# Optimization experiments

Measured on AMD Instinct MI355X. Metric: run time of the kernel, lower is better.

Reference implementation:

```python
import jax, jax.numpy as jnp
import numpy as np

B, S, H = 2, 2048, 1024
G, HEADS = 4, 16
HPG = HEADS // G          # heads per group = 4
HD = H // HEADS           # head_dim = 64
DG = H // G               # per-group proj dim = 256
SCALE = 1.0 / np.sqrt(HD)


def setup_inputs() -> dict:
    key = jax.random.key(0)
    ks = jax.random.split(key, 6)
    w = 0.02
    return {
        "hidden_states": jax.random.normal(ks[0], (B, S, H), dtype=jnp.float32),
        "Wq": jax.random.normal(ks[1], (G, DG, H), dtype=jnp.float32) * w,
        "bq": jnp.zeros((G, DG), dtype=jnp.float32),
        "Wk": jax.random.normal(ks[2], (G, DG, H), dtype=jnp.float32) * w,
        "bk": jnp.zeros((G, DG), dtype=jnp.float32),
        "Wv": jax.random.normal(ks[3], (G, DG, H), dtype=jnp.float32) * w,
        "bv": jnp.zeros((G, DG), dtype=jnp.float32),
        "Wo": jax.random.normal(ks[4], (H, H), dtype=jnp.float32) * w,
        "bo": jnp.zeros((H,), dtype=jnp.float32),
    }


def _proj_split(x, W, b):
    # x: [B,S,H], W: [G,DG,H], b: [G,DG] -> [B,G,HPG,S,HD]
    y = jnp.einsum("bsh,gdh->bgsd", x, W) + b[None, :, None, :]
    y = y.reshape(x.shape[0], G, x.shape[1], HPG, HD)
    return jnp.transpose(y, (0, 1, 3, 2, 4))


def reference(hidden_states, Wq, bq, Wk, bk, Wv, bv, Wo, bo):
    q = _proj_split(hidden_states, Wq, bq)  # [B,G,HPG,S,HD]
    k = _proj_split(hidden_states, Wk, bk)
    v = _proj_split(hidden_states, Wv, bv)
    scores = jnp.einsum("bghqd,bghkd->bghqk", q, k) * SCALE
    attn = jax.nn.softmax(scores.astype(jnp.float32), axis=-1).astype(v.dtype)
    ctx = jnp.einsum("bghqk,bghkd->bghqd", attn, v)  # [B,G,HPG,S,HD]
    # merge: heads ordered group-major, matching torch cat over group dim
    ctx = jnp.transpose(ctx, (0, 3, 1, 2, 4)).reshape(hidden_states.shape[0], hidden_states.shape[1], H)
    return jnp.einsum("bsh,oh->bso", ctx, Wo) + bo
```

## Files before the change

### kernel.cpp

```cpp
#include <hip/hip_runtime.h>

typedef __bf16 bf16x8 __attribute__((ext_vector_type(8)));
typedef float f32x4 __attribute__((ext_vector_type(4)));
typedef float f32x16 __attribute__((ext_vector_type(16)));
typedef unsigned int uint4v __attribute__((ext_vector_type(4)));
typedef unsigned int uint2v __attribute__((ext_vector_type(2)));

#define LOG2E 1.4426950408889634f

static __device__ __forceinline__ unsigned short f2bf(float f) {
  union { float f; unsigned int u; } c; c.f = f;
  return (unsigned short)((c.u + 0x7fffu + ((c.u >> 16) & 1u)) >> 16);
}

static __device__ __forceinline__ void gload16(const void* g, void* l) {
  __builtin_amdgcn_global_load_lds(
      (const __attribute__((address_space(1))) void*)g,
      (__attribute__((address_space(3))) void*)l, 16, 0, 0);
}

static __device__ __forceinline__ float exp2fast(float x) {
#if __has_builtin(__builtin_amdgcn_exp2f)
  return __builtin_amdgcn_exp2f(x);
#else
  return exp2f(x);
#endif
}

static __device__ __forceinline__ f32x16 mfma32(bf16x8 a, bf16x8 b, f32x16 c) {
  return __builtin_amdgcn_mfma_f32_32x32x16_bf16(a, b, c, 0, 0, 0);
}

static __device__ __forceinline__ unsigned cvt_pk_bf16(float a, float b) {
  unsigned r;
  asm("v_cvt_pk_bf16_f32 %0, %1, %2" : "=v"(r) : "v"(a), "v"(b));
  return r;
}

static __device__ __forceinline__ void pl32_swap(unsigned& a, unsigned& b) {
#if __has_builtin(__builtin_amdgcn_permlane32_swap)
  uint2v r = __builtin_amdgcn_permlane32_swap(a, b, false, false);
  a = r[0]; b = r[1];
#else
  asm volatile("v_permlane32_swap_b32 %0, %1" : "+v"(a), "+v"(b));
#endif
}

__global__ void cvt_all(const float* __restrict__ x,
                        const float* __restrict__ Wq,
                        const float* __restrict__ Wk,
                        const float* __restrict__ Wv,
                        const float* __restrict__ Wo,
                        ushort4* __restrict__ dst) {
  int i = blockIdx.x * 256 + threadIdx.x;
  const float* src;
  int off;
  if (i < 1048576) {
    src = x; off = i;
  } else {
    int t = (i - 1048576) >> 18;
    off = (i - 1048576) & 262143;
    src = (t == 0) ? Wq : (t == 1) ? Wk : (t == 2) ? Wv : Wo;
  }
  float4 f = ((const float4*)src)[off];
  ushort4 o;
  o.x = f2bf(f.x); o.y = f2bf(f.y); o.z = f2bf(f.z); o.w = f2bf(f.w);
  dst[i] = o;
}

__launch_bounds__(256, 4)
__global__ void qkv_gemm(const unsigned short* __restrict__ xb,
                         const unsigned short* __restrict__ wq,
                         const unsigned short* __restrict__ wk,
                         const unsigned short* __restrict__ wv,
                         const float* __restrict__ bq,
                         const float* __restrict__ bk,
                         const float* __restrict__ bv,
                         unsigned short* __restrict__ Qo,
                         unsigned short* __restrict__ Ko,
                         unsigned short* __restrict__ VTo) {
  __shared__ unsigned short As[128 * 64];
  __shared__ unsigned short Bs[128 * 64];
  const int s0 = blockIdx.x * 128;
  const int n0g = blockIdx.y * 128;
  const int qkv = n0g >> 10;
  const int d0 = n0g & 1023;
  const unsigned short* W = (qkv == 0) ? wq : ((qkv == 1) ? wk : wv);
  const float* bias = (qkv == 0) ? bq : ((qkv == 1) ? bk : bv);

  const unsigned short* Aptr; const unsigned short* Bptr;
  int Aoff, Boff;
  if (qkv < 2) { Aptr = W;  Aoff = d0; Bptr = xb; Boff = s0; }
  else         { Aptr = xb; Aoff = s0; Bptr = W;  Boff = d0; }

  const int tid = threadIdx.x;
  const int lane = tid & 63;
  const int wid = tid >> 6;
  const int wm = (wid >> 1) * 64;
  const int wn = (wid & 1) * 64;
  const int lm = lane & 15;
  const int quad = lane >> 4;

  f32x4 acc[4][4] = {};

  for (int kk = 0; kk < 1024; kk += 64) {
#pragma unroll
    for (int t = 0; t < 4; ++t) {
      int i = t * 256 + tid;
      int row = i >> 3, tp = i & 7;
      int seg = tp ^ (row & 7);
      gload16(Aptr + (size_t)(Aoff + row) * 1024 + kk + seg * 8,
              As + (size_t)i * 8);
      gload16(Bptr + (size_t)(Boff + row) * 1024 + kk + seg * 8,
              Bs + (size_t)i * 8);
    }
    __syncthreads();
#pragma unroll
    for (int h = 0; h < 2; ++h) {
      bf16x8 af[4], bff[4];
#pragma unroll
      for (int mt = 0; mt < 4; ++mt) {
        int r = wm + mt * 16 + lm;
        af[mt] = *(const bf16x8*)(As + r * 64 + (((h * 4 + quad) ^ (r & 7)) * 8));
      }
#pragma unroll
      for (int nt = 0; nt < 4; ++nt) {
        int r = wn + nt * 16 + lm;
        bff[nt] = *(const bf16x8*)(Bs + r * 64 + (((h * 4 + quad) ^ (r & 7)) * 8));
      }
#pragma unroll
      for (int mt = 0; mt < 4; ++mt)
#pragma unroll
        for (int nt = 0; nt < 4; ++nt)
          acc[mt][nt] = __builtin_amdgcn_mfma_f32_16x16x32_bf16(
              af[mt], bff[nt], acc[mt][nt], 0, 0, 0);
    }
    __syncthreads();
  }

  if (qkv < 2) {
    unsigned short* OUT = (qkv == 0) ? Qo : Ko;
    const float scale = (qkv == 0) ? (0.125f * LOG2E) : 1.0f;
#pragma unroll
    for (int mt = 0; mt < 4; ++mt) {
      const int d = d0 + wm + mt * 16 + quad * 4;
      const int g = d >> 8, hpg = (d >> 6) & 3, hd = d & 63;
      const float4 bb = *(const float4*)(bias + d);
#pragma unroll
      for (int nt = 0; nt < 4; ++nt) {
        const int srow = s0 + wn + nt * 16 + lm;
        const int bidx = srow >> 11, s = srow & 2047;
        const int head = (bidx * 4 + g) * 4 + hpg;
        ushort4 o;
        o.x = f2bf((acc[mt][nt][0] + bb.x) * scale);
        o.y = f2bf((acc[mt][nt][1] + bb.y) * scale);
        o.z = f2bf((acc[mt][nt][2] + bb.z) * scale);
        o.w = f2bf((acc[mt][nt][3] + bb.w) * scale);
        *(ushort4*)(OUT + (size_t)head * 131072 + (size_t)s * 64 + hd) = o;
      }
    }
  } else {
#pragma unroll
    for (int nt = 0; nt < 4; ++nt) {
      const int d = d0 + wn + nt * 16 + lm;
      const int g = d >> 8, hpg = (d >> 6) & 3, hd = d & 63;
      const float bb = bias[d];
#pragma unroll
      for (int mt = 0; mt < 4; ++mt) {
        const int sbase = s0 + wm + mt * 16 + quad * 4;
        const int bidx = sbase >> 11, s = sbase & 2047;
        const int head = (bidx * 4 + g) * 4 + hpg;
        ushort4 o;
        o.x = f2bf(acc[mt][nt][0] + bb);
        o.y = f2bf(acc[mt][nt][1] + bb);
        o.z = f2bf(acc[mt][nt][2] + bb);
        o.w = f2bf(acc[mt][nt][3] + bb);
        *(ushort4*)(VTo + (size_t)head * 131072 + (size_t)hd * 2048 + s) = o;
      }
    }
  }
}

static __device__ __forceinline__ void stage_kv(
    const unsigned short* Kh, const unsigned short* Vh, int kv0,
    unsigned short* ksl, unsigned short* vsl, int tid) {
#pragma unroll
  for (int t = 0; t < 4; ++t) {
    int i = t * 256 + tid;
    int r = i >> 3, j = i & 7;
    gload16(Kh + (size_t)(kv0 + r) * 64 + ((j ^ (r & 7)) << 3),
            ksl + (size_t)i * 8);
  }
#pragma unroll
  for (int t = 0; t < 4; ++t) {
    int i = t * 256 + tid;
    int r = i >> 4, j = i & 15;
    gload16(Vh + (size_t)r * 2048 + kv0 + ((j ^ (r & 15)) << 3),
            vsl + (size_t)i * 8);
  }
}

__launch_bounds__(256, 2)
__global__ void attn_kernel(const unsigned short* __restrict__ Q,
                            const unsigned short* __restrict__ K,
                            const unsigned short* __restrict__ VT,
                            unsigned short* __restrict__ ctx) {
  __shared__ __align__(16) unsigned char smem[65536];

  const int f = blockIdx.x;
  const int xcd = f & 7;
  const int idx = f >> 3;
  const int head = xcd * 4 + (idx & 3);
  const int q0 = (idx >> 2) * 128;
  const int b = head >> 4;
  const int colbase = (head & 15) * 64;

  const unsigned short* Qh = Q + (size_t)head * 131072;
  const unsigned short* Kh = K + (size_t)head * 131072;
  const unsigned short* Vh = VT + (size_t)head * 131072;

  const int tid = threadIdx.x;
  const int lane = tid & 63;
  const int w = tid >> 6;
  const int wq = w & 1;
  const int wkv = w >> 1;
  const int l31 = lane & 31;
  const int hi = lane >> 5;

  stage_kv(Kh, Vh, 0, (unsigned short*)smem,
           (unsigned short*)(smem + 32768), tid);

  bf16x8 qf[2][4];
#pragma unroll
  for (int qs = 0; qs < 2; ++qs) {
    const size_t qrow = (size_t)(q0 + wq * 64 + qs * 32 + l31);
#pragma unroll
    for (int s = 0; s < 4; ++s)
      qf[qs][s] = *(const bf16x8*)(Qh + qrow * 64 + s * 16 + hi * 8);
  }

  int koff[2][4];
#pragma unroll
  for (int kb = 0; kb < 2; ++kb) {
    const int row = wkv * 64 + kb * 32 + l31;
#pragma unroll
    for (int s = 0; s < 4; ++s) {
      const int c = s * 2 + hi;
      koff[kb][s] = row * 64 + ((c ^ (row & 7)) << 3);
    }
  }
  int voff[2][2][2];
#pragma unroll
  for (int kb = 0; kb < 2; ++kb)
#pragma unroll
    for (int db = 0; db < 2; ++db) {
      const int row = db * 32 + l31;
#pragma unroll
      for (int t = 0; t < 2; ++t) {
        const int c = wkv * 8 + kb * 4 + t * 2 + hi;
        voff[kb][db][t] = row * 128 + ((c ^ (row & 15)) << 3);
      }
    }

  __syncthreads();

  float psum[2] = {0.f, 0.f};
  f32x16 oacc[2][2] = {};

  for (int it = 0; it < 16; ++it) {
    const int buf = it & 1;
    const unsigned short* kbuf = (const unsigned short*)(smem + buf * 16384);
    const unsigned short* vbuf =
        (const unsigned short*)(smem + 32768 + buf * 16384);
    if (it < 15)
      stage_kv(Kh, Vh, (it + 1) * 128,
               (unsigned short*)(smem + (buf ^ 1) * 16384),
               (unsigned short*)(smem + 32768 + (buf ^ 1) * 16384), tid);

#pragma unroll
    for (int kb = 0; kb < 2; ++kb) {
      bf16x8 kf[4], vf[2][2];
#pragma unroll
      for (int s = 0; s < 4; ++s)
        kf[s] = *(const bf16x8*)(kbuf + koff[kb][s]);
#pragma unroll
      for (int db = 0; db < 2; ++db)
#pragma unroll
        for (int t = 0; t < 2; ++t)
          vf[db][t] = *(const bf16x8*)(vbuf + voff[kb][db][t]);

#pragma unroll
      for (int qs = 0; qs < 2; ++qs) {
        f32x16 sc = {};
#pragma unroll
        for (int s = 0; s < 4; ++s)
          sc = mfma32(kf[s], qf[qs][s], sc);

        float e[16];
#pragma unroll
        for (int r = 0; r < 16; ++r) e[r] = exp2fast(sc[r]);
        {
          float t0 = (e[0] + e[1]) + (e[2] + e[3]);
          float t1 = (e[4] + e[5]) + (e[6] + e[7]);
          float t2 = (e[8] + e[9]) + (e[10] + e[11]);
          float t3 = (e[12] + e[13]) + (e[14] + e[15]);
          psum[qs] += (t0 + t1) + (t2 + t3);
        }
        unsigned p[8];
#pragma unroll
        for (int j = 0; j < 8; ++j) p[j] = cvt_pk_bf16(e[2 * j], e[2 * j + 1]);
        pl32_swap(p[0], p[2]); pl32_swap(p[1], p[3]);
        pl32_swap(p[4], p[6]); pl32_swap(p[5], p[7]);
        uint4v u0 = {p[0], p[1], p[2], p[3]};
        uint4v u1 = {p[4], p[5], p[6], p[7]};
        const bf16x8 B0 = __builtin_bit_cast(bf16x8, u0);
        const bf16x8 B1 = __builtin_bit_cast(bf16x8, u1);
#pragma unroll
        for (int db = 0; db < 2; ++db) {
          oacc[qs][db] = mfma32(vf[db][0], B0, oacc[qs][db]);
          oacc[qs][db] = mfma32(vf[db][1], B1, oacc[qs][db]);
        }
      }
    }
    __syncthreads();
  }

#pragma unroll
  for (int qs = 0; qs < 2; ++qs)
    psum[qs] += __shfl_xor(psum[qs], 32, 64);

  float* red = (float*)smem;
  float* psred = (float*)(smem + 34816);
  if (wkv == 1) {
#pragma unroll
    for (int qs = 0; qs < 2; ++qs) {
      const int qi = wq * 64 + qs * 32 + l31;
      if (hi == 0) psred[qi] = psum[qs];
#pragma unroll
      for (int db = 0; db < 2; ++db)
#pragma unroll
        for (int g = 0; g < 4; ++g) {
          f32x4 ov;
          ov[0] = oacc[qs][db][4 * g + 0];
          ov[1] = oacc[qs][db][4 * g + 1];
          ov[2] = oacc[qs][db][4 * g + 2];
          ov[3] = oacc[qs][db][4 * g + 3];
          *(f32x4*)(red + qi * 68 + db * 32 + g * 8 + hi * 4) = ov;
        }
    }
  }
  __syncthreads();
  if (wkv == 0) {
#pragma unroll
    for (int qs = 0; qs < 2; ++qs) {
      const int qi = wq * 64 + qs * 32 + l31;
      const float inv = 1.0f / (psum[qs] + psred[qi]);
      const size_t row = (size_t)(b * 2048 + q0 + qi);
#pragma unroll
      for (int db = 0; db < 2; ++db)
#pragma unroll
        for (int g = 0; g < 4; ++g) {
          f32x4 o = *(const f32x4*)(red + qi * 68 + db * 32 + g * 8 + hi * 4);
          ushort4 st;
          st.x = f2bf((o[0] + oacc[qs][db][4 * g + 0]) * inv);
          st.y = f2bf((o[1] + oacc[qs][db][4 * g + 1]) * inv);
          st.z = f2bf((o[2] + oacc[qs][db][4 * g + 2]) * inv);
          st.w = f2bf((o[3] + oacc[qs][db][4 * g + 3]) * inv);
          *(ushort4*)(ctx + row * 1024 + colbase + db * 32 + g * 8 + hi * 4) =
              st;
        }
    }
  }
}

__launch_bounds__(256, 4)
__global__ void out_gemm(const unsigned short* __restrict__ A,
                         const unsigned short* __restrict__ Wb,
                         const float* __restrict__ bo,
                         float* __restrict__ out) {
  __shared__ unsigned short As[128 * 64];
  __shared__ unsigned short Bs[64 * 64];
  const int s0 = blockIdx.x * 64;
  const int o0 = blockIdx.y * 128;

  const int tid = threadIdx.x;
  const int lane = tid & 63;
  const int wid = tid >> 6;
  const int wm = (wid >> 1) * 64;
  const int wn = (wid & 1) * 32;
  const int lm = lane & 15;
  const int quad = lane >> 4;

  f32x4 acc[4][2] = {};

  for (int kk = 0; kk < 1024; kk += 64) {
#pragma unroll
    for (int t = 0; t < 4; ++t) {
      int i = t * 256 + tid;
      int row = i >> 3, tp = i & 7;
      int seg = tp ^ (row & 7);
      gload16(Wb + (size_t)(o0 + row) * 1024 + kk + seg * 8, As + (size_t)i * 8);
    }
#pragma unroll
    for (int t = 0; t < 2; ++t) {
      int i = t * 256 + tid;
      int row = i >> 3, tp = i & 7;
      int seg = tp ^ (row & 7);
      gload16(A + (size_t)(s0 + row) * 1024 + kk + seg * 8, Bs + (size_t)i * 8);
    }
    __syncthreads();
#pragma unroll
    for (int h = 0; h < 2; ++h) {
      bf16x8 af[4], bff[2];
#pragma unroll
      for (int mt = 0; mt < 4; ++mt) {
        int r = wm + mt * 16 + lm;
        af[mt] = *(const bf16x8*)(As + r * 64 + (((h * 4 + quad) ^ (r & 7)) * 8));
      }
#pragma unroll
      for (int nt = 0; nt < 2; ++nt) {
        int r = wn + nt * 16 + lm;
        bff[nt] = *(const bf16x8*)(Bs + r * 64 + (((h * 4 + quad) ^ (r & 7)) * 8));
      }
#pragma unroll
      for (int mt = 0; mt < 4; ++mt)
#pragma unroll
        for (int nt = 0; nt < 2; ++nt)
          acc[mt][nt] = __builtin_amdgcn_mfma_f32_16x16x32_bf16(
              af[mt], bff[nt], acc[mt][nt], 0, 0, 0);
    }
    __syncthreads();
  }

#pragma unroll
  for (int mt = 0; mt < 4; ++mt) {
    const int o = o0 + wm + mt * 16 + quad * 4;
    const float4 bb = *(const float4*)(bo + o);
#pragma unroll
    for (int nt = 0; nt < 2; ++nt) {
      const int s = s0 + wn + nt * 16 + lm;
      float4 v;
      v.x = acc[mt][nt][0] + bb.x;
      v.y = acc[mt][nt][1] + bb.y;
      v.z = acc[mt][nt][2] + bb.z;
      v.w = acc[mt][nt][3] + bb.w;
      *(float4*)(out + (size_t)s * 1024 + o) = v;
    }
  }
}

extern "C" void kernel_launch(void* const* d_in, const int* in_sizes, int n_in,
                              void* d_out, int out_size, void* d_ws, size_t ws_size,
                              hipStream_t stream) {
  const float* x  = (const float*)d_in[0];
  const float* Wq = (const float*)d_in[1];
  const float* bq = (const float*)d_in[2];
  const float* Wk = (const float*)d_in[3];
  const float* bk = (const float*)d_in[4];
  const float* Wv = (const float*)d_in[5];
  const float* bv = (const float*)d_in[6];
  const float* Wo = (const float*)d_in[7];
  const float* bo = (const float*)d_in[8];
  float* out = (float*)d_out;

  char* ws = (char*)d_ws;
  unsigned short* xb  = (unsigned short*)(ws + 0);
  unsigned short* wqb = (unsigned short*)(ws + 8388608);
  unsigned short* wkb = (unsigned short*)(ws + 10485760);
  unsigned short* wvb = (unsigned short*)(ws + 12582912);
  unsigned short* wob = (unsigned short*)(ws + 14680064);
  unsigned short* Qb  = (unsigned short*)(ws + 16777216);
  unsigned short* Kb  = (unsigned short*)(ws + 25165824);
  unsigned short* VTb = (unsigned short*)(ws + 33554432);
  unsigned short* ctxb= (unsigned short*)(ws + 41943040);
  if (ws_size < 50331648) return;

  cvt_all<<<8192, 256, 0, stream>>>(x, Wq, Wk, Wv, Wo, (ushort4*)ws);
  qkv_gemm<<<dim3(32, 24), 256, 0, stream>>>(xb, wqb, wkb, wvb, bq, bk, bv,
                                             Qb, Kb, VTb);
  attn_kernel<<<dim3(512), 256, 0, stream>>>(Qb, Kb, VTb, ctxb);
  out_gemm<<<dim3(64, 8), 256, 0, stream>>>(ctxb, wob, bo, out);
}
```

Baseline: 175.6 us.

## Halve attention tiles to 64 queries and 64 KV rows, raise occupancy

The attention kernel now handles 64 query rows per block instead of 128 and stages KV in 64-row chunks, halving LDS to 32 KB. The grid doubles to 1024 blocks and launch bounds go to 4 waves per SIMD, aiming for more concurrency and latency hiding. The cost is double the K/V traffic per query, since each KV tile is reused by fewer queries, plus twice as many loop iterations and barriers.

Result: slower. 182.1 us (+3.7%).

```diff
diff --git a/kernel.cpp b/kernel.cpp
--- a/kernel.cpp
+++ b/kernel.cpp
@@ -181,37 +181,37 @@
   }
 }
 
-static __device__ __forceinline__ void stage_kv(
+static __device__ __forceinline__ void stage_kv64(
     const unsigned short* Kh, const unsigned short* Vh, int kv0,
     unsigned short* ksl, unsigned short* vsl, int tid) {
 #pragma unroll
-  for (int t = 0; t < 4; ++t) {
+  for (int t = 0; t < 2; ++t) {
     int i = t * 256 + tid;
     int r = i >> 3, j = i & 7;
     gload16(Kh + (size_t)(kv0 + r) * 64 + ((j ^ (r & 7)) << 3),
             ksl + (size_t)i * 8);
   }
 #pragma unroll
-  for (int t = 0; t < 4; ++t) {
+  for (int t = 0; t < 2; ++t) {
     int i = t * 256 + tid;
-    int r = i >> 4, j = i & 15;
-    gload16(Vh + (size_t)r * 2048 + kv0 + ((j ^ (r & 15)) << 3),
+    int r = i >> 3, j = i & 7;
+    gload16(Vh + (size_t)r * 2048 + kv0 + ((j ^ (r & 7)) << 3),
             vsl + (size_t)i * 8);
   }
 }
 
-__launch_bounds__(256, 2)
+__launch_bounds__(256, 4)
 __global__ void attn_kernel(const unsigned short* __restrict__ Q,
                             const unsigned short* __restrict__ K,
                             const unsigned short* __restrict__ VT,
                             unsigned short* __restrict__ ctx) {
-  __shared__ __align__(16) unsigned char smem[65536];
+  __shared__ __align__(16) unsigned char smem[32768];
 
   const int f = blockIdx.x;
   const int xcd = f & 7;
   const int idx = f >> 3;
   const int head = xcd * 4 + (idx & 3);
-  const int q0 = (idx >> 2) * 128;
+  const int q0 = (idx >> 2) * 64;
   const int b = head >> 4;
   const int colbase = (head & 15) * 64;
 
@@ -227,149 +227,129 @@
   const int l31 = lane & 31;
   const int hi = lane >> 5;
 
-  stage_kv(Kh, Vh, 0, (unsigned short*)smem,
-           (unsigned short*)(smem + 32768), tid);
-
-  bf16x8 qf[2][4];
-#pragma unroll
-  for (int qs = 0; qs < 2; ++qs) {
-    const size_t qrow = (size_t)(q0 + wq * 64 + qs * 32 + l31);
+  stage_kv64(Kh, Vh, 0, (unsigned short*)smem,
+             (unsigned short*)(smem + 16384), tid);
+
+  bf16x8 qf[4];
+  {
+    const size_t qrow = (size_t)(q0 + wq * 32 + l31);
 #pragma unroll
     for (int s = 0; s < 4; ++s)
-      qf[qs][s] = *(const bf16x8*)(Qh + qrow * 64 + s * 16 + hi * 8);
-  }
-
-  int koff[2][4];
-#pragma unroll
-  for (int kb = 0; kb < 2; ++kb) {
-    const int row = wkv * 64 + kb * 32 + l31;
+      qf[s] = *(const bf16x8*)(Qh + qrow * 64 + s * 16 + hi * 8);
+  }
+
+  int koff[4];
+  {
+    const int r = wkv * 32 + l31;
 #pragma unroll
     for (int s = 0; s < 4; ++s) {
       const int c = s * 2 + hi;
-      koff[kb][s] = row * 64 + ((c ^ (row & 7)) << 3);
-    }
-  }
-  int voff[2][2][2];
-#pragma unroll
-  for (int kb = 0; kb < 2; ++kb)
+      koff[s] = r * 64 + ((c ^ (r & 7)) << 3);
+    }
+  }
+  int voff[2][2];
+#pragma unroll
+  for (int db = 0; db < 2; ++db) {
+    const int r = db * 32 + l31;
+#pragma unroll
+    for (int t = 0; t < 2; ++t) {
+      const int c = wkv * 4 + t * 2 + hi;
+      voff[db][t] = r * 64 + ((c ^ (r & 7)) << 3);
+    }
+  }
+
+  __syncthreads();
+
+  float psum = 0.f;
+  f32x16 oacc[2] = {};
+
+  for (int it = 0; it < 32; ++it) {
+    const int buf = it & 1;
+    const unsigned short* kbuf = (const unsigned short*)(smem + buf * 8192);
+    const unsigned short* vbuf =
+        (const unsigned short*)(smem + 16384 + buf * 8192);
+    if (it < 31)
+      stage_kv64(Kh, Vh, (it + 1) * 64,
+                 (unsigned short*)(smem + (buf ^ 1) * 8192),
+                 (unsigned short*)(smem + 16384 + (buf ^ 1) * 8192), tid);
+
+    bf16x8 kf[4], vf[2][2];
+#pragma unroll
+    for (int s = 0; s < 4; ++s)
+      kf[s] = *(const bf16x8*)(kbuf + koff[s]);
+#pragma unroll
+    for (int db = 0; db < 2; ++db)
+#pragma unroll
+      for (int t = 0; t < 2; ++t)
+        vf[db][t] = *(const bf16x8*)(vbuf + voff[db][t]);
+
+    f32x16 sc = {};
+#pragma unroll
+    for (int s = 0; s < 4; ++s)
+      sc = mfma32(kf[s], qf[s], sc);
+
+    float e[16];
+#pragma unroll
+    for (int r = 0; r < 16; ++r) e[r] = exp2fast(sc[r]);
+    {
+      float t0 = (e[0] + e[1]) + (e[2] + e[3]);
+      float t1 = (e[4] + e[5]) + (e[6] + e[7]);
+      float t2 = (e[8] + e[9]) + (e[10] + e[11]);
+      float t3 = (e[12] + e[13]) + (e[14] + e[15]);
+      psum += (t0 + t1) + (t2 + t3);
+    }
+    unsigned p[8];
+#pragma unroll
+    for (int j = 0; j < 8; ++j) p[j] = cvt_pk_bf16(e[2 * j], e[2 * j + 1]);
+    pl32_swap(p[0], p[2]); pl32_swap(p[1], p[3]);
+    pl32_swap(p[4], p[6]); pl32_swap(p[5], p[7]);
+    uint4v u0 = {p[0], p[1], p[2], p[3]};
+    uint4v u1 = {p[4], p[5], p[6], p[7]};
+    const bf16x8 B0 = __builtin_bit_cast(bf16x8, u0);
+    const bf16x8 B1 = __builtin_bit_cast(bf16x8, u1);
 #pragma unroll
     for (int db = 0; db < 2; ++db) {
-      const int row = db * 32 + l31;
-#pragma unroll
-      for (int t = 0; t < 2; ++t) {
-        const int c = wkv * 8 + kb * 4 + t * 2 + hi;
-        voff[kb][db][t] = row * 128 + ((c ^ (row & 15)) << 3);
-      }
-    }
-
-  __syncthreads();
-
-  float psum[2] = {0.f, 0.f};
-  f32x16 oacc[2][2] = {};
-
-  for (int it = 0; it < 16; ++it) {
-    const int buf = it & 1;
-    const unsigned short* kbuf = (const unsigned short*)(smem + buf * 16384);
-    const unsigned short* vbuf =
-        (const unsigned short*)(smem + 32768 + buf * 16384);
-    if (it < 15)
-      stage_kv(Kh, Vh, (it + 1) * 128,
-               (unsigned short*)(smem + (buf ^ 1) * 16384),
-               (unsigned short*)(smem + 32768 + (buf ^ 1) * 16384), tid);
-
-#pragma unroll
-    for (int kb = 0; kb < 2; ++kb) {
-      bf16x8 kf[4], vf[2][2];
-#pragma unroll
-      for (int s = 0; s < 4; ++s)
-        kf[s] = *(const bf16x8*)(kbuf + koff[kb][s]);
-#pragma unroll
-      for (int db = 0; db < 2; ++db)
-#pragma unroll
-        for (int t = 0; t < 2; ++t)
-          vf[db][t] = *(const bf16x8*)(vbuf + voff[kb][db][t]);
-
-#pragma unroll
-      for (int qs = 0; qs < 2; ++qs) {
-        f32x16 sc = {};
-#pragma unroll
-        for (int s = 0; s < 4; ++s)
-          sc = mfma32(kf[s], qf[qs][s], sc);
-
-        float e[16];
-#pragma unroll
-        for (int r = 0; r < 16; ++r) e[r] = exp2fast(sc[r]);
-        {
-          float t0 = (e[0] + e[1]) + (e[2] + e[3]);
-          float t1 = (e[4] + e[5]) + (e[6] + e[7]);
-          float t2 = (e[8] + e[9]) + (e[10] + e[11]);
-          float t3 = (e[12] + e[13]) + (e[14] + e[15]);
-          psum[qs] += (t0 + t1) + (t2 + t3);
-        }
-        unsigned p[8];
-#pragma unroll
-        for (int j = 0; j < 8; ++j) p[j] = cvt_pk_bf16(e[2 * j], e[2 * j + 1]);
-        pl32_swap(p[0], p[2]); pl32_swap(p[1], p[3]);
-        pl32_swap(p[4], p[6]); pl32_swap(p[5], p[7]);
-        uint4v u0 = {p[0], p[1], p[2], p[3]};
-        uint4v u1 = {p[4], p[5], p[6], p[7]};
-        const bf16x8 B0 = __builtin_bit_cast(bf16x8, u0);
-        const bf16x8 B1 = __builtin_bit_cast(bf16x8, u1);
-#pragma unroll
-        for (int db = 0; db < 2; ++db) {
-          oacc[qs][db] = mfma32(vf[db][0], B0, oacc[qs][db]);
-          oacc[qs][db] = mfma32(vf[db][1], B1, oacc[qs][db]);
-        }
-      }
+      oacc[db] = mfma32(vf[db][0], B0, oacc[db]);
+      oacc[db] = mfma32(vf[db][1], B1, oacc[db]);
     }
     __syncthreads();
   }
 
-#pragma unroll
-  for (int qs = 0; qs < 2; ++qs)
-    psum[qs] += __shfl_xor(psum[qs], 32, 64);
+  psum += __shfl_xor(psum, 32, 64);
 
   float* red = (float*)smem;
-  float* psred = (float*)(smem + 34816);
+  float* psred = (float*)(smem + 17408);
+  const int qi = wq * 32 + l31;
   if (wkv == 1) {
-#pragma unroll
-    for (int qs = 0; qs < 2; ++qs) {
-      const int qi = wq * 64 + qs * 32 + l31;
-      if (hi == 0) psred[qi] = psum[qs];
-#pragma unroll
-      for (int db = 0; db < 2; ++db)
-#pragma unroll
-        for (int g = 0; g < 4; ++g) {
-          f32x4 ov;
-          ov[0] = oacc[qs][db][4 * g + 0];
-          ov[1] = oacc[qs][db][4 * g + 1];
-          ov[2] = oacc[qs][db][4 * g + 2];
-          ov[3] = oacc[qs][db][4 * g + 3];
-          *(f32x4*)(red + qi * 68 + db * 32 + g * 8 + hi * 4) = ov;
-        }
-    }
+    if (hi == 0) psred[qi] = psum;
+#pragma unroll
+    for (int db = 0; db < 2; ++db)
+#pragma unroll
+      for (int g = 0; g < 4; ++g) {
+        f32x4 ov;
+        ov[0] = oacc[db][4 * g + 0];
+        ov[1] = oacc[db][4 * g + 1];
+        ov[2] = oacc[db][4 * g + 2];
+        ov[3] = oacc[db][4 * g + 3];
+        *(f32x4*)(red + qi * 68 + db * 32 + g * 8 + hi * 4) = ov;
+      }
   }
   __syncthreads();
   if (wkv == 0) {
-#pragma unroll
-    for (int qs = 0; qs < 2; ++qs) {
-      const int qi = wq * 64 + qs * 32 + l31;
-      const float inv = 1.0f / (psum[qs] + psred[qi]);
-      const size_t row = (size_t)(b * 2048 + q0 + qi);
-#pragma unroll
-      for (int db = 0; db < 2; ++db)
-#pragma unroll
-        for (int g = 0; g < 4; ++g) {
-          f32x4 o = *(const f32x4*)(red + qi * 68 + db * 32 + g * 8 + hi * 4);
-          ushort4 st;
-          st.x = f2bf((o[0] + oacc[qs][db][4 * g + 0]) * inv);
-          st.y = f2bf((o[1] + oacc[qs][db][4 * g + 1]) * inv);
-          st.z = f2bf((o[2] + oacc[qs][db][4 * g + 2]) * inv);
-          st.w = f2bf((o[3] + oacc[qs][db][4 * g + 3]) * inv);
-          *(ushort4*)(ctx + row * 1024 + colbase + db * 32 + g * 8 + hi * 4) =
-              st;
-        }
-    }
+    const float inv = 1.0f / (psum + psred[qi]);
+    const size_t row = (size_t)(b * 2048 + q0 + qi);
+#pragma unroll
+    for (int db = 0; db < 2; ++db)
+#pragma unroll
+      for (int g = 0; g < 4; ++g) {
+        f32x4 o = *(const f32x4*)(red + qi * 68 + db * 32 + g * 8 + hi * 4);
+        ushort4 st;
+        st.x = f2bf((o[0] + oacc[db][4 * g + 0]) * inv);
+        st.y = f2bf((o[1] + oacc[db][4 * g + 1]) * inv);
+        st.z = f2bf((o[2] + oacc[db][4 * g + 2]) * inv);
+        st.w = f2bf((o[3] + oacc[db][4 * g + 3]) * inv);
+        *(ushort4*)(ctx + row * 1024 + colbase + db * 32 + g * 8 + hi * 4) = st;
+      }
   }
 }
 
@@ -478,6 +458,6 @@
   cvt_all<<<8192, 256, 0, stream>>>(x, Wq, Wk, Wv, Wo, (ushort4*)ws);
   qkv_gemm<<<dim3(32, 24), 256, 0, stream>>>(xb, wqb, wkb, wvb, bq, bk, bv,
                                              Qb, Kb, VTb);
-  attn_kernel<<<dim3(512), 256, 0, stream>>>(Qb, Kb, VTb, ctxb);
+  attn_kernel<<<dim3(1024), 256, 0, stream>>>(Qb, Kb, VTb, ctxb);
   out_gemm<<<dim3(64, 8), 256, 0, stream>>>(ctxb, wob, bo, out);
 }
```

## Re-swizzle K/V shared tiles with 512-byte row groups and prioritize MFMA issue

Applied to the files above, without the earlier changes.

Changes the LDS layout of the staged K and V tiles. Several logical rows are packed into 512-byte super-rows and 16-byte chunks are XOR-swizzled across 32 positions, with the per-lane read offsets recomputed to match. The goal is to remove LDS bank conflicts on the ds_read_b128 fragment loads. It also raises wave priority with s_setprio around the MFMA blocks so matrix instructions from different waves interleave better with the exp and softmax VALU work. The new swizzle has to line up exactly between the staging writes and the fragment reads, or results will be wrong.

Result: no change. 178.1 us (+1.4%).

```diff
diff --git a/kernel.cpp b/kernel.cpp
--- a/kernel.cpp
+++ b/kernel.cpp
@@ -187,16 +187,18 @@
 #pragma unroll
   for (int t = 0; t < 4; ++t) {
     int i = t * 256 + tid;
-    int r = i >> 3, j = i & 7;
-    gload16(Kh + (size_t)(kv0 + r) * 64 + ((j ^ (r & 7)) << 3),
-            ksl + (size_t)i * 8);
+    int rr = i >> 5, ccp = i & 31;
+    int cc = ccp ^ (rr & 31);
+    int r = rr * 4 + (cc >> 3), c = cc & 7;
+    gload16(Kh + (size_t)(kv0 + r) * 64 + c * 8, ksl + (size_t)i * 8);
   }
 #pragma unroll
   for (int t = 0; t < 4; ++t) {
     int i = t * 256 + tid;
-    int r = i >> 4, j = i & 15;
-    gload16(Vh + (size_t)r * 2048 + kv0 + ((j ^ (r & 15)) << 3),
-            vsl + (size_t)i * 8);
+    int rr = i >> 5, ccp = i & 31;
+    int cc = ccp ^ (rr & 31);
+    int r = rr * 2 + (cc >> 4), c = cc & 15;
+    gload16(Vh + (size_t)r * 2048 + kv0 + c * 8, vsl + (size_t)i * 8);
   }
 }
 
@@ -242,11 +244,12 @@
   int koff[2][4];
 #pragma unroll
   for (int kb = 0; kb < 2; ++kb) {
-    const int row = wkv * 64 + kb * 32 + l31;
+    const int r = wkv * 64 + kb * 32 + l31;
+    const int rr = r >> 2;
 #pragma unroll
     for (int s = 0; s < 4; ++s) {
-      const int c = s * 2 + hi;
-      koff[kb][s] = row * 64 + ((c ^ (row & 7)) << 3);
+      const int cc = (r & 3) * 8 + s * 2 + hi;
+      koff[kb][s] = rr * 256 + ((cc ^ (rr & 31)) << 3);
     }
   }
   int voff[2][2][2];
@@ -254,11 +257,12 @@
   for (int kb = 0; kb < 2; ++kb)
 #pragma unroll
     for (int db = 0; db < 2; ++db) {
-      const int row = db * 32 + l31;
+      const int r = db * 32 + l31;
+      const int rr = r >> 1;
 #pragma unroll
       for (int t = 0; t < 2; ++t) {
-        const int c = wkv * 8 + kb * 4 + t * 2 + hi;
-        voff[kb][db][t] = row * 128 + ((c ^ (row & 15)) << 3);
+        const int cc = (r & 1) * 16 + wkv * 8 + kb * 4 + t * 2 + hi;
+        voff[kb][db][t] = rr * 256 + ((cc ^ (rr & 31)) << 3);
       }
     }
 
@@ -292,9 +296,11 @@
 #pragma unroll
       for (int qs = 0; qs < 2; ++qs) {
         f32x16 sc = {};
+        __builtin_amdgcn_s_setprio(1);
 #pragma unroll
         for (int s = 0; s < 4; ++s)
           sc = mfma32(kf[s], qf[qs][s], sc);
+        __builtin_amdgcn_s_setprio(0);
 
         float e[16];
 #pragma unroll
@@ -315,11 +321,13 @@
         uint4v u1 = {p[4], p[5], p[6], p[7]};
         const bf16x8 B0 = __builtin_bit_cast(bf16x8, u0);
         const bf16x8 B1 = __builtin_bit_cast(bf16x8, u1);
+        __builtin_amdgcn_s_setprio(1);
 #pragma unroll
         for (int db = 0; db < 2; ++db) {
           oacc[qs][db] = mfma32(vf[db][0], B0, oacc[qs][db]);
           oacc[qs][db] = mfma32(vf[db][1], B1, oacc[qs][db]);
         }
+        __builtin_amdgcn_s_setprio(0);
       }
     }
     __syncthreads();
```
